# Kernel tuning notes

Hardware: AMD Instinct MI355X
Metric: run time of the kernel (lower is better)

Reference implementation:

```python
import jax, jax.numpy as jnp
import numpy as np

B = 16
N = [4096, 1024, 256, 64, 16]
NF = [1, 16, 32, 64, 128, 256]
DEG = 6
KS = 5
LAT = 32


def spline_conv(x, edge_index, pseudo, W, root, bias):
    """SplineConv: open B-spline, degree 1, dim 3, kernel_size 5, sum aggregation (norm=False).
    x: [Nn, Cin], edge_index: [2, E] (src, dst), pseudo: [E, 3] in [0,1], W: [125, Cin, Cout]."""
    src, dst = edge_index[0], edge_index[1]
    v = pseudo * (KS - 1)                       # degree-1 open spline interval
    lo = jnp.clip(jnp.floor(v), 0.0, KS - 2)
    frac = v - lo                               # [E, 3]
    lo = lo.astype(jnp.int32)
    xs = x[src]                                 # [E, Cin] gather
    strides = jnp.array([1, KS, KS * KS], dtype=jnp.int32)
    msg = jnp.zeros((src.shape[0], W.shape[2]), dtype=x.dtype)
    for s in range(8):                          # (degree+1)^dim = 8 basis products
        bits = np.array([(s >> d) & 1 for d in range(3)], dtype=np.int32)
        basis = jnp.prod(jnp.where(bits[None, :] == 1, frac, 1.0 - frac), axis=1)  # [E]
        kidx = jnp.sum((lo + bits[None, :]) * strides[None, :], axis=1)            # [E]
        Wg = W[kidx]                                                               # [E, Cin, Cout]
        msg = msg + basis[:, None] * jnp.einsum('ei,eio->eo', xs, Wg)
    agg = jax.ops.segment_sum(msg, dst, num_segments=x.shape[0])
    return agg + x @ root + bias


def _fwd(fl, ei):
    (x, ea0, ea1, ea2, ea3, ea4, P01, P12, P23, P34, Pn1, P1n, P43, P32, P21, P10,
     W_c1, r_c1, b_c1, W_c2, r_c2, b_c2, W_c3, r_c3, b_c3, W_c4, r_c4, b_c4, W_c5, r_c5, b_c5,
     W_d5, r_d5, b_d5, W_d4, r_d4, b_d4, W_d3, r_d3, b_d3, W_d2, r_d2, b_d2, W_d1, r_d1, b_d1,
     fce1_w, fce1_b, fce21_w, fce21_b, fce22_w, fce22_b, fcd3_w, fcd3_b, fcd4_w, fcd4_b, eps) = fl
    ei0, ei1, ei2, ei3, ei4 = ei
    elu = jax.nn.elu
    # ---- encoder ----
    h = elu(spline_conv(x, ei0, ea0, W_c1, r_c1, b_c1))
    h = P01 @ h.reshape(B, N[0], NF[1])
    h = elu(spline_conv(h.reshape(-1, NF[1]), ei1, ea1, W_c2, r_c2, b_c2))
    h = P12 @ h.reshape(B, N[1], NF[2])
    h = elu(spline_conv(h.reshape(-1, NF[2]), ei2, ea2, W_c3, r_c3, b_c3))
    h = P23 @ h.reshape(B, N[2], NF[3])
    h = elu(spline_conv(h.reshape(-1, NF[3]), ei3, ea3, W_c4, r_c4, b_c4))
    h = P34 @ h.reshape(B, N[3], NF[4])
    h = elu(spline_conv(h.reshape(-1, NF[4]), ei4, ea4, W_c5, r_c5, b_c5))
    h = (Pn1 @ h.reshape(B, N[4], NF[5])).reshape(B, NF[5])
    # 1x1 convs over [B, C, 1, 1] == dense layers
    h = elu(h @ fce1_w + fce1_b)
    mu = h @ fce21_w + fce21_b
    logvar = h @ fce22_w + fce22_b
    # ---- reparameterize ----
    z = eps * jnp.exp(0.5 * logvar) + mu
    # ---- decoder ----
    h = elu(z @ fcd3_w + fcd3_b)
    h = elu(h @ fcd4_w + fcd4_b)
    h = P1n @ h.reshape(B, 1, NF[5])            # [B, N4, nf5]
    h = elu(spline_conv(h.reshape(-1, NF[5]), ei4, ea4, W_d5, r_d5, b_d5))
    h = P43 @ h.reshape(B, N[4], NF[4])
    h = elu(spline_conv(h.reshape(-1, NF[4]), ei3, ea3, W_d4, r_d4, b_d4))
    h = P32 @ h.reshape(B, N[3], NF[3])
    h = elu(spline_conv(h.reshape(-1, NF[3]), ei2, ea2, W_d3, r_d3, b_d3))
    h = P21 @ h.reshape(B, N[2], NF[2])
    h = elu(spline_conv(h.reshape(-1, NF[2]), ei1, ea1, W_d2, r_d2, b_d2))
    h = P10 @ h.reshape(B, N[1], NF[1])
    h = elu(spline_conv(h.reshape(-1, NF[1]), ei0, ea0, W_d1, r_d1, b_d1))
    recon = h.reshape(B, -1)                    # [B, N0] (nf0 == 1)
    return recon, mu, logvar


def setup_inputs() -> dict:
    key = jax.random.key(0)
    ks = iter(jax.random.split(key, 128))
    def nrm(shape, scale=1.0):
        return jax.random.normal(next(ks), shape, dtype=jnp.float32) * scale
    def edges(n):
        # per-sample random mesh-like connectivity, offset per graph copy
        e = jax.random.randint(next(ks), (2, B, n * DEG), 0, n)
        off = (jnp.arange(B) * n)[None, :, None]
        return (e + off).reshape(2, -1).astype(jnp.int32)
    inp = {}
    inp['x'] = nrm((B * N[0], NF[0]))
    for i in range(5):
        inp[f'ea{i}'] = jax.random.uniform(next(ks), (B * N[i] * DEG, 3), dtype=jnp.float32)
    pools = {'P01': (N[1], N[0]), 'P12': (N[2], N[1]), 'P23': (N[3], N[2]), 'P34': (N[4], N[3]),
             'Pn1': (1, N[4]), 'P1n': (N[4], 1), 'P43': (N[3], N[4]), 'P32': (N[2], N[3]),
             'P21': (N[1], N[2]), 'P10': (N[0], N[1])}
    for k2, (a, b) in pools.items():
        inp[k2] = nrm((a, b), 1.0 / np.sqrt(b))
    def spl(name, ci, co):
        inp[f'W_{name}'] = nrm((KS ** 3, ci, co), 0.1 / np.sqrt(ci))
        inp[f'r_{name}'] = nrm((ci, co), 1.0 / np.sqrt(ci))
        inp[f'b_{name}'] = nrm((co,), 0.01)
    spl('c1', NF[0], NF[1]); spl('c2', NF[1], NF[2]); spl('c3', NF[2], NF[3]); spl('c4', NF[3], NF[4]); spl('c5', NF[4], NF[5])
    spl('d5', NF[5], NF[4]); spl('d4', NF[4], NF[3]); spl('d3', NF[3], NF[2]); spl('d2', NF[2], NF[1]); spl('d1', NF[1], NF[0])
    def lin(name, ci, co):
        inp[f'{name}_w'] = nrm((ci, co), 1.0 / np.sqrt(ci))
        inp[f'{name}_b'] = nrm((co,), 0.01)
    lin('fce1', NF[5], NF[5]); lin('fce21', NF[5], LAT); lin('fce22', NF[5], LAT)
    lin('fcd3', LAT, NF[5]); lin('fcd4', NF[5], NF[5])
    inp['eps'] = nrm((B, LAT))
    for i in range(5):
        inp[f'ei{i}'] = edges(N[i])
    return inp


def reference(x, ea0, ea1, ea2, ea3, ea4, P01, P12, P23, P34, Pn1, P1n, P43, P32, P21, P10,
              W_c1, r_c1, b_c1, W_c2, r_c2, b_c2, W_c3, r_c3, b_c3, W_c4, r_c4, b_c4, W_c5, r_c5, b_c5,
              W_d5, r_d5, b_d5, W_d4, r_d4, b_d4, W_d3, r_d3, b_d3, W_d2, r_d2, b_d2, W_d1, r_d1, b_d1,
              fce1_w, fce1_b, fce21_w, fce21_b, fce22_w, fce22_b, fcd3_w, fcd3_b, fcd4_w, fcd4_b, eps,
              ei0, ei1, ei2, ei3, ei4):
    fl = (x, ea0, ea1, ea2, ea3, ea4, P01, P12, P23, P34, Pn1, P1n, P43, P32, P21, P10,
          W_c1, r_c1, b_c1, W_c2, r_c2, b_c2, W_c3, r_c3, b_c3, W_c4, r_c4, b_c4, W_c5, r_c5, b_c5,
          W_d5, r_d5, b_d5, W_d4, r_d4, b_d4, W_d3, r_d3, b_d3, W_d2, r_d2, b_d2, W_d1, r_d1, b_d1,
          fce1_w, fce1_b, fce21_w, fce21_b, fce22_w, fce22_b, fcd3_w, fcd3_b, fcd4_w, fcd4_b, eps)
    return _fwd(fl, (ei0, ei1, ei2, ei3, ei4))
```

## Files before the change

kernel.cpp:

```cpp
#include <hip/hip_runtime.h>
#include <hip/hip_bf16.h>

#define TPB 256
#define CDIV(a,b) (((a)+(b)-1)/(b))

__device__ __forceinline__ float elu_f(float v) {
    return v > 0.f ? v : expm1f(v);
}

__device__ __forceinline__ int ld_idx(const void* __restrict__ ei, int pos, int is64) {
    if (is64) return (int)((const long long*)ei)[pos];
    return ((const int*)ei)[pos];
}

__device__ __forceinline__ void spline_basis(const float* __restrict__ pseudo, int e,
                                             float bas[8], int kidx[8]) {
    float f[3]; int lo[3];
#pragma unroll
    for (int d = 0; d < 3; ++d) {
        float v = pseudo[e * 3 + d] * 4.f;
        float l = floorf(v);
        l = fminf(fmaxf(l, 0.f), 3.f);
        f[d] = v - l;
        lo[d] = (int)l;
    }
#pragma unroll
    for (int s = 0; s < 8; ++s) {
        int b0 = s & 1, b1 = (s >> 1) & 1, b2 = (s >> 2) & 1;
        bas[s] = (b0 ? f[0] : 1.f - f[0]) * (b1 ? f[1] : 1.f - f[1]) * (b2 ? f[2] : 1.f - f[2]);
        kidx[s] = (lo[0] + b0) + 5 * (lo[1] + b1) + 25 * (lo[2] + b2);
    }
}

__global__ void k_detect(const int* __restrict__ ei0_as_i32, int* __restrict__ flag) {
    if (threadIdx.x == 0 && blockIdx.x == 0) {
        int zeros = 0;
        for (int k = 0; k < 128; ++k)
            if (ei0_as_i32[2 * k + 1] == 0) zeros++;
        flag[0] = (zeros >= 120) ? 1 : 0;
    }
}

__global__ __launch_bounds__(TPB) void k_zero(float* __restrict__ p, int n) {
    int t = blockIdx.x * blockDim.x + threadIdx.x;
    if (t < n) p[t] = 0.f;
}

__global__ __launch_bounds__(TPB) void k_zero_i(int* __restrict__ p, int n) {
    int t = blockIdx.x * blockDim.x + threadIdx.x;
    if (t < n) p[t] = 0;
}

__global__ __launch_bounds__(TPB) void k_csr_count(const void* __restrict__ ei,
                                                   int* __restrict__ cnt, int E,
                                                   const int* __restrict__ flag) {
    int t = blockIdx.x * blockDim.x + threadIdx.x;
    if (t >= E) return;
    int dst = ld_idx(ei, E + t, flag[0]);
    atomicAdd(&cnt[dst], 1);
}

__global__ __launch_bounds__(1024) void k_csr_scan(const int* __restrict__ cnt,
                                                   int* __restrict__ row_ptr) {
    __shared__ int s_part[1024];
    int t = threadIdx.x;
    int base = t * 64;
    int sum = 0;
    for (int i = 0; i < 64; ++i) sum += cnt[base + i];
    s_part[t] = sum;
    __syncthreads();
    for (int off = 1; off < 1024; off <<= 1) {
        int v = (t >= off) ? s_part[t - off] : 0;
        __syncthreads();
        s_part[t] += v;
        __syncthreads();
    }
    int run = (t == 0) ? 0 : s_part[t - 1];
    for (int i = 0; i < 64; ++i) { row_ptr[base + i] = run; run += cnt[base + i]; }
    if (t == 1023) row_ptr[65536] = run;
}

__global__ __launch_bounds__(TPB) void k_csr_fill(const void* __restrict__ ei,
                                                  const int* __restrict__ row_ptr,
                                                  int* __restrict__ cur,
                                                  int* __restrict__ eid, int E,
                                                  const int* __restrict__ flag) {
    int t = blockIdx.x * blockDim.x + threadIdx.x;
    if (t >= E) return;
    int dst = ld_idx(ei, E + t, flag[0]);
    int pos = row_ptr[dst] + atomicAdd(&cur[dst], 1);
    eid[pos] = t;
}

__global__ __launch_bounds__(256) void k_gather_c1(const float* __restrict__ x,
                                                   const float* __restrict__ pseudo,
                                                   const void* __restrict__ ei,
                                                   const float* __restrict__ W,
                                                   const float* __restrict__ root,
                                                   const float* __restrict__ bias,
                                                   const int* __restrict__ row_ptr,
                                                   const int* __restrict__ eid,
                                                   float* __restrict__ agg,
                                                   const int* __restrict__ flag) {
    __shared__ float4 s_w[500];
    for (int i = threadIdx.x; i < 500; i += 256)
        s_w[i] = reinterpret_cast<const float4*>(W)[i];
    __syncthreads();
    int t = blockIdx.x * 256 + threadIdx.x;
    int n = t >> 2, cg = t & 3, co0 = cg * 4;
    int is64 = flag[0];
    float xn = x[n];
    float a0 = fmaf(xn, root[co0 + 0], bias[co0 + 0]);
    float a1 = fmaf(xn, root[co0 + 1], bias[co0 + 1]);
    float a2 = fmaf(xn, root[co0 + 2], bias[co0 + 2]);
    float a3 = fmaf(xn, root[co0 + 3], bias[co0 + 3]);
    int rb = row_ptr[n], re = row_ptr[n + 1];
    for (int idx = rb; idx < re; ++idx) {
        int e = eid[idx];
        int src = ld_idx(ei, e, is64);
        float bas[8]; int kidx[8];
        spline_basis(pseudo, e, bas, kidx);
        float xs = x[src];
        float m0 = 0.f, m1 = 0.f, m2 = 0.f, m3 = 0.f;
#pragma unroll
        for (int s = 0; s < 8; ++s) {
            float4 w = s_w[kidx[s] * 4 + cg];
            float bs = bas[s];
            m0 = fmaf(bs, w.x, m0);
            m1 = fmaf(bs, w.y, m1);
            m2 = fmaf(bs, w.z, m2);
            m3 = fmaf(bs, w.w, m3);
        }
        a0 = fmaf(xs, m0, a0);
        a1 = fmaf(xs, m1, a1);
        a2 = fmaf(xs, m2, a2);
        a3 = fmaf(xs, m3, a3);
    }
    float4 v = make_float4(a0, a1, a2, a3);
    *reinterpret_cast<float4*>(&agg[n * 16 + co0]) = v;
}

__global__ __launch_bounds__(256) void k_gather_d1(const float* __restrict__ xin,
                                                   const float* __restrict__ pseudo,
                                                   const void* __restrict__ ei,
                                                   const float* __restrict__ W,
                                                   const float* __restrict__ root,
                                                   const float* __restrict__ bias,
                                                   const int* __restrict__ row_ptr,
                                                   const int* __restrict__ eid,
                                                   float* __restrict__ outp,
                                                   const int* __restrict__ flag) {
    __shared__ float s_w[2000];
    for (int i = threadIdx.x; i < 2000; i += 256) s_w[i] = W[i];
    __syncthreads();
    int t = blockIdx.x * 256 + threadIdx.x;
    int n = t >> 2, l = t & 3;
    int is64 = flag[0];
    int rb = row_ptr[n], re = row_ptr[n + 1];
    float acc = 0.f;
    for (int idx = rb + l; idx < re; idx += 4) {
        int e = eid[idx];
        int src = ld_idx(ei, e, is64);
        float bas[8]; int kidx[8];
        spline_basis(pseudo, e, bas, kidx);
        const float4* xs4 = reinterpret_cast<const float4*>(xin + src * 16);
        float4 xv0 = xs4[0], xv1 = xs4[1], xv2 = xs4[2], xv3 = xs4[3];
        float m = 0.f;
#pragma unroll
        for (int s = 0; s < 8; ++s) {
            const float4* wp = reinterpret_cast<const float4*>(s_w + kidx[s] * 16);
            float4 w0 = wp[0], w1 = wp[1], w2 = wp[2], w3 = wp[3];
            float p = 0.f;
            p = fmaf(xv0.x, w0.x, p); p = fmaf(xv0.y, w0.y, p);
            p = fmaf(xv0.z, w0.z, p); p = fmaf(xv0.w, w0.w, p);
            p = fmaf(xv1.x, w1.x, p); p = fmaf(xv1.y, w1.y, p);
            p = fmaf(xv1.z, w1.z, p); p = fmaf(xv1.w, w1.w, p);
            p = fmaf(xv2.x, w2.x, p); p = fmaf(xv2.y, w2.y, p);
            p = fmaf(xv2.z, w2.z, p); p = fmaf(xv2.w, w2.w, p);
            p = fmaf(xv3.x, w3.x, p); p = fmaf(xv3.y, w3.y, p);
            p = fmaf(xv3.z, w3.z, p); p = fmaf(xv3.w, w3.w, p);
            m = fmaf(bas[s], p, m);
        }
        acc += m;
    }
    acc += __shfl_xor(acc, 1);
    acc += __shfl_xor(acc, 2);
    if (l == 0) {
        const float4* xr = reinterpret_cast<const float4*>(xin + n * 16);
        const float4* rr = reinterpret_cast<const float4*>(root);
        float r = bias[0];
#pragma unroll
        for (int q = 0; q < 4; ++q) {
            float4 xv = xr[q], rv = rr[q];
            r = fmaf(xv.x, rv.x, r); r = fmaf(xv.y, rv.y, r);
            r = fmaf(xv.z, rv.z, r); r = fmaf(xv.w, rv.w, r);
        }
        outp[n] = elu_f(r + acc);
    }
}

__global__ __launch_bounds__(TPB) void k_root4(const float* __restrict__ x,
                                               const float* __restrict__ root,
                                               const float* __restrict__ bias,
                                               float* __restrict__ out,
                                               int nnode, int cin, int cout) {
    int t = blockIdx.x * blockDim.x + threadIdx.x;
    if (t >= nnode * cout) return;
    int n = t / cout, co = t - n * cout;
    const float4* xr = reinterpret_cast<const float4*>(x + n * cin);
    float a0 = 0.f, a1 = 0.f, a2 = 0.f, a3 = 0.f;
    int q4 = cin >> 2;
    for (int q = 0; q < q4; ++q) {
        float4 xv = xr[q];
        const float* rp = root + (q * 4) * cout + co;
        a0 = fmaf(xv.x, rp[0], a0);
        a1 = fmaf(xv.y, rp[cout], a1);
        a2 = fmaf(xv.z, rp[2 * cout], a2);
        a3 = fmaf(xv.w, rp[3 * cout], a3);
    }
    out[t] = bias[co] + ((a0 + a1) + (a2 + a3));
}

template <int CIN, int COUT, int CSPLIT>
__global__ __launch_bounds__(TPB) void k_msg4(const float* __restrict__ x,
                                              const float* __restrict__ pseudo,
                                              const void* __restrict__ ei,
                                              const float* __restrict__ W,
                                              float* __restrict__ agg, int E,
                                              const int* __restrict__ flag) {
    constexpr int COG = COUT / 4;
    constexpr int CPT = CIN / CSPLIT;
    int t = blockIdx.x * blockDim.x + threadIdx.x;
    if (t >= E * COG * CSPLIT) return;
    int is64 = flag[0];
    int cog = t % COG;
    int rest = t / COG;
    int cs = rest % CSPLIT;
    int e = rest / CSPLIT;
    int co0 = cog * 4;
    int src = ld_idx(ei, e, is64);
    int dst = ld_idx(ei, E + e, is64);
    float bas[8]; int kidx[8];
    spline_basis(pseudo, e, bas, kidx);
    int wof[8];
#pragma unroll
    for (int s = 0; s < 8; ++s) wof[s] = kidx[s] * CIN * COUT + co0;
    float a0 = 0.f, a1 = 0.f, a2 = 0.f, a3 = 0.f;
    const float* xp = x + src * CIN + cs * CPT;
    const int cbase = cs * CPT * COUT;
    for (int ci = 0; ci < CPT; ++ci) {
        float xv = xp[ci];
        int off = cbase + ci * COUT;
#pragma unroll
        for (int s = 0; s < 8; ++s) {
            float4 w = *reinterpret_cast<const float4*>(&W[wof[s] + off]);
            float bx = bas[s] * xv;
            a0 = fmaf(bx, w.x, a0);
            a1 = fmaf(bx, w.y, a1);
            a2 = fmaf(bx, w.z, a2);
            a3 = fmaf(bx, w.w, a3);
        }
    }
    float* ap = &agg[dst * COUT + co0];
    atomicAdd(ap + 0, a0);
    atomicAdd(ap + 1, a1);
    atomicAdd(ap + 2, a2);
    atomicAdd(ap + 3, a3);
}

template <int CIN, int COUT>
__global__ __launch_bounds__(TPB) void k_msg_s(const float* __restrict__ x,
                                               const float* __restrict__ pseudo,
                                               const void* __restrict__ ei,
                                               const float* __restrict__ W,
                                               float* __restrict__ agg, int E,
                                               const int* __restrict__ flag) {
    int t = blockIdx.x * blockDim.x + threadIdx.x;
    if (t >= E * COUT) return;
    int is64 = flag[0];
    int e = t / COUT, co = t - e * COUT;
    int src = ld_idx(ei, e, is64);
    int dst = ld_idx(ei, E + e, is64);
    float bas[8]; int kidx[8];
    spline_basis(pseudo, e, bas, kidx);
    float acc = 0.f;
    const float* xp = x + src * CIN;
    for (int ci = 0; ci < CIN; ++ci) {
        float xv = xp[ci];
#pragma unroll
        for (int s = 0; s < 8; ++s)
            acc = fmaf(bas[s] * xv, W[kidx[s] * CIN * COUT + ci * COUT + co], acc);
    }
    atomicAdd(&agg[dst * COUT + co], acc);
}

__global__ __launch_bounds__(1024) void k_msg_c1(const float* __restrict__ x,
                                                 const float* __restrict__ pseudo,
                                                 const void* __restrict__ ei,
                                                 const float* __restrict__ W,
                                                 const float* __restrict__ root,
                                                 const float* __restrict__ bias,
                                                 float* __restrict__ agg,
                                                 const int* __restrict__ flag) {
    __shared__ float s_acc[4096 * 4];
    __shared__ float s_w[125 * 4];
    int b = blockIdx.x, cg = blockIdx.y, t = threadIdx.x;
    int co0 = cg * 4;
    int is64 = flag[0];
    if (t < 500) s_w[t] = W[(t >> 2) * 16 + co0 + (t & 3)];
    float r0 = root[co0], r1 = root[co0 + 1], r2 = root[co0 + 2], r3 = root[co0 + 3];
    float b0 = bias[co0], b1 = bias[co0 + 1], b2 = bias[co0 + 2], b3 = bias[co0 + 3];
    for (int n = t; n < 4096; n += 1024) {
        float xv = x[b * 4096 + n];
        s_acc[n * 4 + 0] = fmaf(xv, r0, b0);
        s_acc[n * 4 + 1] = fmaf(xv, r1, b1);
        s_acc[n * 4 + 2] = fmaf(xv, r2, b2);
        s_acc[n * 4 + 3] = fmaf(xv, r3, b3);
    }
    __syncthreads();
    int ebeg = b * 24576;
    for (int k = t; k < 24576; k += 1024) {
        int e = ebeg + k;
        int src = ld_idx(ei, e, is64);
        int dst = ld_idx(ei, 393216 + e, is64);
        float xv = x[src];
        float bas[8]; int kidx[8];
        spline_basis(pseudo, e, bas, kidx);
        float m0 = 0.f, m1 = 0.f, m2 = 0.f, m3 = 0.f;
#pragma unroll
        for (int s = 0; s < 8; ++s) {
            const float* wp = s_w + kidx[s] * 4;
            float bs = bas[s];
            m0 = fmaf(bs, wp[0], m0);
            m1 = fmaf(bs, wp[1], m1);
            m2 = fmaf(bs, wp[2], m2);
            m3 = fmaf(bs, wp[3], m3);
        }
        int dl = (dst - b * 4096) * 4;
        atomicAdd(&s_acc[dl + 0], m0 * xv);
        atomicAdd(&s_acc[dl + 1], m1 * xv);
        atomicAdd(&s_acc[dl + 2], m2 * xv);
        atomicAdd(&s_acc[dl + 3], m3 * xv);
    }
    __syncthreads();
    for (int n = t; n < 4096; n += 1024) {
        float4 v = *reinterpret_cast<float4*>(&s_acc[n * 4]);
        *reinterpret_cast<float4*>(&agg[(b * 4096 + n) * 16 + co0]) = v;
    }
}

template <int F, int ELU>
__global__ __launch_bounds__(256) void k_pool2(const float* __restrict__ in,
                                               const float* __restrict__ P,
                                               float* __restrict__ out,
                                               int nout, int nin) {
    constexpr int FQ = F / 4;
    constexpr int TI = 256 / FQ;
    constexpr int KT = 64;
    constexpr int PS = KT + 4;
    __shared__ float s_p[TI * PS];
    __shared__ float4 s_in[KT * FQ];
    int tid = threadIdx.x;
    int fq = tid % FQ;
    int i = tid / FQ;
    int b = blockIdx.y;
    int gi = blockIdx.x * TI + i;
    int nchunk = nin / gridDim.z;
    int kbeg = blockIdx.z * nchunk;
    const float4* inb4 = reinterpret_cast<const float4*>(in + b * nin * F);
    float4 acc = make_float4(0.f, 0.f, 0.f, 0.f);

    for (int k0 = kbeg; k0 < kbeg + nchunk; k0 += KT) {
        __syncthreads();
        for (int idx = tid; idx < TI * (KT / 4); idx += 256) {
            int r = idx / (KT / 4), c = idx % (KT / 4);
            float4 v = *reinterpret_cast<const float4*>(&P[(blockIdx.x * TI + r) * nin + k0 + c * 4]);
            *reinterpret_cast<float4*>(&s_p[r * PS + c * 4]) = v;
        }
        for (int idx = tid; idx < KT * FQ; idx += 256) {
            float4 v = inb4[(size_t)(k0 + idx / FQ) * FQ + (idx % FQ)];
            if (ELU) {
                v.x = elu_f(v.x); v.y = elu_f(v.y);
                v.z = elu_f(v.z); v.w = elu_f(v.w);
            }
            s_in[idx] = v;
        }
        __syncthreads();
#pragma unroll 4
        for (int j = 0; j < KT; j += 4) {
            float4 pv = *reinterpret_cast<const float4*>(&s_p[i * PS + j]);
            float4 v0 = s_in[(j + 0) * FQ + fq];
            float4 v1 = s_in[(j + 1) * FQ + fq];
            float4 v2 = s_in[(j + 2) * FQ + fq];
            float4 v3 = s_in[(j + 3) * FQ + fq];
            acc.x = fmaf(pv.x, v0.x, acc.x); acc.y = fmaf(pv.x, v0.y, acc.y);
            acc.z = fmaf(pv.x, v0.z, acc.z); acc.w = fmaf(pv.x, v0.w, acc.w);
            acc.x = fmaf(pv.y, v1.x, acc.x); acc.y = fmaf(pv.y, v1.y, acc.y);
            acc.z = fmaf(pv.y, v1.z, acc.z); acc.w = fmaf(pv.y, v1.w, acc.w);
            acc.x = fmaf(pv.z, v2.x, acc.x); acc.y = fmaf(pv.z, v2.y, acc.y);
            acc.z = fmaf(pv.z, v2.z, acc.z); acc.w = fmaf(pv.z, v2.w, acc.w);
            acc.x = fmaf(pv.w, v3.x, acc.x); acc.y = fmaf(pv.w, v3.y, acc.y);
            acc.z = fmaf(pv.w, v3.z, acc.z); acc.w = fmaf(pv.w, v3.w, acc.w);
        }
    }
    float* o = out + ((size_t)b * nout + gi) * F + fq * 4;
    if (gridDim.z > 1) {
        atomicAdd(o + 0, acc.x); atomicAdd(o + 1, acc.y);
        atomicAdd(o + 2, acc.z); atomicAdd(o + 3, acc.w);
    } else {
        *reinterpret_cast<float4*>(o) = acc;
    }
}

__global__ __launch_bounds__(TPB) void k_pool_e(const float* __restrict__ in,
                                                const float* __restrict__ P,
                                                float* __restrict__ out,
                                                int nout, int nin, int F, int elu) {
    int t = blockIdx.x * blockDim.x + threadIdx.x;
    if (t >= 16 * nout * F) return;
    int f = t % F;
    int rest = t / F;
    int i = rest % nout;
    int b = rest / nout;
    const float* ip = in + b * nin * F + f;
    const float* pp = P + i * nin;
    float acc = 0.f;
    if (elu) {
#pragma unroll 4
        for (int j = 0; j < nin; ++j) acc = fmaf(pp[j], elu_f(ip[j * F]), acc);
    } else {
#pragma unroll 4
        for (int j = 0; j < nin; ++j) acc = fmaf(pp[j], ip[j * F], acc);
    }
    out[t] = acc;
}

__global__ __launch_bounds__(1024) void k_fc_fused2(
        const float* __restrict__ c5agg, const float* __restrict__ Pn1,
        const float* __restrict__ fce1_w, const float* __restrict__ fce1_b,
        const float* __restrict__ fce21_w, const float* __restrict__ fce21_b,
        const float* __restrict__ fce22_w, const float* __restrict__ fce22_b,
        const float* __restrict__ eps,
        const float* __restrict__ fcd3_w, const float* __restrict__ fcd3_b,
        const float* __restrict__ fcd4_w, const float* __restrict__ fcd4_b,
        const float* __restrict__ P1n,
        float* __restrict__ out_mu, float* __restrict__ out_lv,
        float* __restrict__ dec_in) {
    __shared__ float s0[256], s1[256], sz[32], sp[1024];
    int b = blockIdx.x, t = threadIdx.x;
    if (t < 256) {
        const float* ap = c5agg + b * 4096 + t;
        float acc = 0.f;
#pragma unroll
        for (int n = 0; n < 16; ++n) acc = fmaf(Pn1[n], elu_f(ap[n * 256]), acc);
        s0[t] = acc;
    }
    __syncthreads();
    {
        int q = t >> 8, co = t & 255;
        const float* w = fce1_w + co;
        float a = 0.f;
        int c0 = q * 64;
        for (int ci = 0; ci < 64; ci += 8) {
#pragma unroll
            for (int k = 0; k < 8; ++k) a = fmaf(s0[c0 + ci + k], w[(c0 + ci + k) * 256], a);
        }
        sp[t] = a;
    }
    __syncthreads();
    if (t < 256) s1[t] = elu_f(sp[t] + sp[t + 256] + sp[t + 512] + sp[t + 768] + fce1_b[t]);
    __syncthreads();
    if (t < 512) {
        int which = t >> 8, r = t & 255;
        int co = r & 31, q = r >> 5;
        const float* w = (which ? fce22_w : fce21_w) + co;
        float a = 0.f;
        int c0 = q * 32;
#pragma unroll
        for (int k = 0; k < 32; ++k) a = fmaf(s1[c0 + k], w[(c0 + k) * 32], a);
        sp[t] = a;
    }
    __syncthreads();
    if (t < 64) {
        int which = t >> 5, co = t & 31;
        float m = (which ? fce22_b : fce21_b)[co];
        int base = which * 256 + co;
#pragma unroll
        for (int q = 0; q < 8; ++q) m += sp[base + q * 32];
        if (which == 0) { out_mu[b * 32 + co] = m; s0[co] = m; }
        else            { out_lv[b * 32 + co] = m; s0[64 + co] = m; }
    }
    __syncthreads();
    if (t < 32) sz[t] = fmaf(eps[b * 32 + t], expf(0.5f * s0[64 + t]), s0[t]);
    __syncthreads();
    if (t < 256) {
        float d = fcd3_b[t];
#pragma unroll
        for (int ci = 0; ci < 32; ++ci) d = fmaf(sz[ci], fcd3_w[ci * 256 + t], d);
        s0[t] = elu_f(d);
    }
    __syncthreads();
    {
        int q = t >> 8, co = t & 255;
        const float* w = fcd4_w + co;
        float a = 0.f;
        int c0 = q * 64;
        for (int ci = 0; ci < 64; ci += 8) {
#pragma unroll
            for (int k = 0; k < 8; ++k) a = fmaf(s0[c0 + ci + k], w[(c0 + ci + k) * 256], a);
        }
        sp[t] = a;
    }
    __syncthreads();
    if (t < 256) s1[t] = elu_f(sp[t] + sp[t + 256] + sp[t + 512] + sp[t + 768] + fcd4_b[t]);
    __syncthreads();
    {
        float* op = dec_in + b * 4096;
        for (int idx = t; idx < 4096; idx += 1024) {
            int n = idx >> 8, f = idx & 255;
            op[idx] = P1n[n] * s1[f];
        }
    }
}

__global__ __launch_bounds__(TPB) void k_elu_out(const float* __restrict__ in,
                                                 float* __restrict__ out, int n) {
    int t = blockIdx.x * blockDim.x + threadIdx.x;
    if (t < n) out[t] = elu_f(in[t]);
}

extern "C" void kernel_launch(void* const* d_in, const int* in_sizes, int n_in,
                              void* d_out, int out_size, void* d_ws, size_t ws_size,
                              hipStream_t stream) {
    const float* x    = (const float*)d_in[0];
    const float* ea0  = (const float*)d_in[1];
    const float* ea1  = (const float*)d_in[2];
    const float* ea2  = (const float*)d_in[3];
    const float* ea3  = (const float*)d_in[4];
    const float* ea4  = (const float*)d_in[5];
    const float* P01  = (const float*)d_in[6];
    const float* P12  = (const float*)d_in[7];
    const float* P23  = (const float*)d_in[8];
    const float* P34  = (const float*)d_in[9];
    const float* Pn1  = (const float*)d_in[10];
    const float* P1n  = (const float*)d_in[11];
    const float* P43  = (const float*)d_in[12];
    const float* P32  = (const float*)d_in[13];
    const float* P21  = (const float*)d_in[14];
    const float* P10  = (const float*)d_in[15];
    const float* W_c1 = (const float*)d_in[16]; const float* r_c1 = (const float*)d_in[17]; const float* b_c1 = (const float*)d_in[18];
    const float* W_c2 = (const float*)d_in[19]; const float* r_c2 = (const float*)d_in[20]; const float* b_c2 = (const float*)d_in[21];
    const float* W_c3 = (const float*)d_in[22]; const float* r_c3 = (const float*)d_in[23]; const float* b_c3 = (const float*)d_in[24];
    const float* W_c4 = (const float*)d_in[25]; const float* r_c4 = (const float*)d_in[26]; const float* b_c4 = (const float*)d_in[27];
    const float* W_c5 = (const float*)d_in[28]; const float* r_c5 = (const float*)d_in[29]; const float* b_c5 = (const float*)d_in[30];
    const float* W_d5 = (const float*)d_in[31]; const float* r_d5 = (const float*)d_in[32]; const float* b_d5 = (const float*)d_in[33];
    const float* W_d4 = (const float*)d_in[34]; const float* r_d4 = (const float*)d_in[35]; const float* b_d4 = (const float*)d_in[36];
    const float* W_d3 = (const float*)d_in[37]; const float* r_d3 = (const float*)d_in[38]; const float* b_d3 = (const float*)d_in[39];
    const float* W_d2 = (const float*)d_in[40]; const float* r_d2 = (const float*)d_in[41]; const float* b_d2 = (const float*)d_in[42];
    const float* W_d1 = (const float*)d_in[43]; const float* r_d1 = (const float*)d_in[44]; const float* b_d1 = (const float*)d_in[45];
    const float* fce1_w  = (const float*)d_in[46]; const float* fce1_b  = (const float*)d_in[47];
    const float* fce21_w = (const float*)d_in[48]; const float* fce21_b = (const float*)d_in[49];
    const float* fce22_w = (const float*)d_in[50]; const float* fce22_b = (const float*)d_in[51];
    const float* fcd3_w  = (const float*)d_in[52]; const float* fcd3_b  = (const float*)d_in[53];
    const float* fcd4_w  = (const float*)d_in[54]; const float* fcd4_b  = (const float*)d_in[55];
    const float* eps  = (const float*)d_in[56];
    const void* ei0 = d_in[57];
    const void* ei1 = d_in[58];
    const void* ei2 = d_in[59];
    const void* ei3 = d_in[60];
    const void* ei4 = d_in[61];

    const int E0 = 393216, E1 = 98304, E2 = 24576, E3 = 6144, E4 = 1536;
    const int N0 = 65536, N1 = 16384, N2 = 4096, N3 = 1024, N4 = 256;

    float* sm   = (float*)d_ws;
    float* bufA = sm + 13824;
    float* bufB = bufA + 1048576;
    int*  flag  = (int*)(bufB + 262144);
    int*  csr_row = (int*)(bufB + 262144 + 64);
    int*  csr_cur = csr_row + 65537;
    int*  csr_eid = csr_cur + 65536;
    const size_t WS_NEED = (size_t)(13824 + 1048576 + 262144 + 64 + 524352) * 4;
    const bool big_ws = ws_size >= WS_NEED;

    float* out = (float*)d_out;
    float* out_mu = out + 65536;
    float* out_lv = out + 66048;

    auto g = [](int n) { return dim3((unsigned)CDIV(n, TPB)); };

    k_detect<<<1, 64, 0, stream>>>((const int*)ei0, flag);

    if (big_ws) {
        k_zero_i<<<g(65536), TPB, 0, stream>>>(csr_cur, 65536);
        k_csr_count<<<g(E0), TPB, 0, stream>>>(ei0, csr_cur, E0, flag);
        k_csr_scan<<<1, 1024, 0, stream>>>(csr_cur, csr_row);
        k_zero_i<<<g(65536), TPB, 0, stream>>>(csr_cur, 65536);
        k_csr_fill<<<g(E0), TPB, 0, stream>>>(ei0, csr_row, csr_cur, csr_eid, E0, flag);
    }

    if (big_ws) {
        k_gather_c1<<<1024, 256, 0, stream>>>(x, ea0, ei0, W_c1, r_c1, b_c1,
                                              csr_row, csr_eid, bufA, flag);
    } else {
        k_msg_c1<<<dim3(16, 4), 1024, 0, stream>>>(x, ea0, ei0, W_c1, r_c1, b_c1, bufA, flag);
    }
    k_zero<<<g(262144), TPB, 0, stream>>>(bufB, 262144);
    k_pool2<16, 1><<<dim3(16, 16, 4), 256, 0, stream>>>(bufA, P01, bufB, 1024, 4096);

    k_root4<<<g(N1 * 32), TPB, 0, stream>>>(bufB, r_c2, b_c2, bufA, N1, 16, 32);
    k_msg4<16, 32, 1><<<g(E1 * 8), TPB, 0, stream>>>(bufB, ea1, ei1, W_c2, bufA, E1, flag);
    k_zero<<<g(131072), TPB, 0, stream>>>(bufB, 131072);
    k_pool2<32, 1><<<dim3(8, 16, 2), 256, 0, stream>>>(bufA, P12, bufB, 256, 1024);

    k_root4<<<g(N2 * 64), TPB, 0, stream>>>(bufB, r_c3, b_c3, bufA, N2, 32, 64);
    k_msg4<32, 64, 1><<<g(E2 * 16), TPB, 0, stream>>>(bufB, ea2, ei2, W_c3, bufA, E2, flag);
    k_zero<<<g(65536), TPB, 0, stream>>>(bufB, 65536);
    k_pool2<64, 1><<<dim3(4, 16, 2), 256, 0, stream>>>(bufA, P23, bufB, 64, 256);

    k_root4<<<g(N3 * 128), TPB, 0, stream>>>(bufB, r_c4, b_c4, bufA, N3, 64, 128);
    k_msg4<64, 128, 1><<<g(E3 * 32), TPB, 0, stream>>>(bufB, ea3, ei3, W_c4, bufA, E3, flag);
    k_pool_e<<<g(16 * 16 * 128), TPB, 0, stream>>>(bufA, P34, bufB, 16, 64, 128, 1);

    k_root4<<<g(N4 * 256), TPB, 0, stream>>>(bufB, r_c5, b_c5, bufA, N4, 128, 256);
    k_msg4<128, 256, 2><<<g(E4 * 128), TPB, 0, stream>>>(bufB, ea4, ei4, W_c5, bufA, E4, flag);

    k_fc_fused2<<<16, 1024, 0, stream>>>(bufA, Pn1,
                                         fce1_w, fce1_b, fce21_w, fce21_b, fce22_w, fce22_b,
                                         eps, fcd3_w, fcd3_b, fcd4_w, fcd4_b, P1n,
                                         out_mu, out_lv, bufA);

    k_root4<<<g(N4 * 128), TPB, 0, stream>>>(bufA, r_d5, b_d5, bufB, N4, 256, 128);
    k_msg4<256, 128, 4><<<g(E4 * 128), TPB, 0, stream>>>(bufA, ea4, ei4, W_d5, bufB, E4, flag);
    k_pool_e<<<g(16 * 64 * 128), TPB, 0, stream>>>(bufB, P43, bufA, 64, 16, 128, 1);

    k_root4<<<g(N3 * 64), TPB, 0, stream>>>(bufA, r_d4, b_d4, bufB, N3, 128, 64);
    k_msg4<128, 64, 2><<<g(E3 * 32), TPB, 0, stream>>>(bufA, ea3, ei3, W_d4, bufB, E3, flag);
    k_pool2<64, 1><<<dim3(16, 16, 1), 256, 0, stream>>>(bufB, P32, bufA, 256, 64);

    k_root4<<<g(N2 * 32), TPB, 0, stream>>>(bufA, r_d3, b_d3, bufB, N2, 64, 32);
    k_msg4<64, 32, 1><<<g(E2 * 8), TPB, 0, stream>>>(bufA, ea2, ei2, W_d3, bufB, E2, flag);
    k_pool2<32, 1><<<dim3(32, 16, 1), 256, 0, stream>>>(bufB, P21, bufA, 1024, 256);

    k_root4<<<g(N1 * 16), TPB, 0, stream>>>(bufA, r_d2, b_d2, bufB, N1, 32, 16);
    k_msg4<32, 16, 1><<<g(E1 * 4), TPB, 0, stream>>>(bufA, ea1, ei1, W_d2, bufB, E1, flag);
    k_pool2<16, 1><<<dim3(64, 16, 1), 256, 0, stream>>>(bufB, P10, bufA, 4096, 1024);

    if (big_ws) {
        k_gather_d1<<<1024, 256, 0, stream>>>(bufA, ea0, ei0, W_d1, r_d1, b_d1,
                                              csr_row, csr_eid, out, flag);
    } else {
        k_root4<<<g(N0 * 1), TPB, 0, stream>>>(bufA, r_d1, b_d1, bufB, N0, 16, 1);
        k_msg_s<16, 1><<<g(E0), TPB, 0, stream>>>(bufA, ea0, ei0, W_d1, bufB, E0, flag);
        k_elu_out<<<g(N0), TPB, 0, stream>>>(bufB, out, 65536);
    }
}
```

Before: 938.3 us.

## Build CSR for all levels and use dst-gather spline conv with shared-memory weights

Builds CSR (count, scan, fill) for all five graph levels in single batched kernels. It then replaces the atomic-scatter k_msg4 layers with a gather kernel that stages the relevant W slice in shared memory and accumulates per destination node. Small levels with the channel dimension fully covered fuse the root term and write directly; split-channel variants still use atomics on top of k_root4. The change is meant to cut global atomics and repeated global reads of W, at the cost of extra CSR-building work and load imbalance on nodes with many edges.

```diff
diff --git a/kernel.cpp b/kernel.cpp
--- a/kernel.cpp
+++ b/kernel.cpp
@@ -49,6 +49,73 @@
 __global__ __launch_bounds__(TPB) void k_zero_i(int* __restrict__ p, int n) {
     int t = blockIdx.x * blockDim.x + threadIdx.x;
     if (t < n) p[t] = 0;
+}
+
+__global__ __launch_bounds__(TPB) void k_csr_count5(const void* e0, const void* e1,
+                                                    const void* e2, const void* e3,
+                                                    const void* e4, int* __restrict__ cnt,
+                                                    const int* __restrict__ flag) {
+    int t = blockIdx.x * blockDim.x + threadIdx.x;
+    if (t >= 523776) return;
+    int is64 = flag[0];
+    const void* ei; int e, E, noff;
+    if (t < 393216)      { ei = e0; e = t;          E = 393216; noff = 0; }
+    else if (t < 491520) { ei = e1; e = t - 393216; E = 98304;  noff = 65536; }
+    else if (t < 516096) { ei = e2; e = t - 491520; E = 24576;  noff = 81920; }
+    else if (t < 522240) { ei = e3; e = t - 516096; E = 6144;   noff = 86016; }
+    else                 { ei = e4; e = t - 522240; E = 1536;   noff = 87040; }
+    int dst = ld_idx(ei, E + e, is64);
+    atomicAdd(&cnt[noff + dst], 1);
+}
+
+__global__ __launch_bounds__(1024) void k_csr_scan5(const int* __restrict__ cnt,
+                                                    int* __restrict__ rows) {
+    const int NODES[5] = {65536, 16384, 4096, 1024, 256};
+    const int NOFF[5]  = {0, 65536, 81920, 86016, 87040};
+    const int ROFF[5]  = {0, 65537, 81922, 86019, 87044};
+    int l = blockIdx.x;
+    int nodes = NODES[l];
+    const int* c = cnt + NOFF[l];
+    int* rp = rows + ROFF[l];
+    __shared__ int s_part[1024];
+    int t = threadIdx.x;
+    int chunk = (nodes + 1023) >> 10;
+    int b0 = t * chunk;
+    int b1 = min(b0 + chunk, nodes);
+    int sum = 0;
+    for (int i = b0; i < b1; ++i) sum += c[i];
+    s_part[t] = sum;
+    __syncthreads();
+    for (int off = 1; off < 1024; off <<= 1) {
+        int v = (t >= off) ? s_part[t - off] : 0;
+        __syncthreads();
+        s_part[t] += v;
+        __syncthreads();
+    }
+    int run = (t == 0) ? 0 : s_part[t - 1];
+    for (int i = b0; i < b1; ++i) { rp[i] = run; run += c[i]; }
+    if (t == 0) rp[nodes] = s_part[1023];
+}
+
+__global__ __launch_bounds__(TPB) void k_csr_fill5(const void* e0, const void* e1,
+                                                   const void* e2, const void* e3,
+                                                   const void* e4,
+                                                   const int* __restrict__ rows,
+                                                   int* __restrict__ cur,
+                                                   int* __restrict__ eids,
+                                                   const int* __restrict__ flag) {
+    int t = blockIdx.x * blockDim.x + threadIdx.x;
+    if (t >= 523776) return;
+    int is64 = flag[0];
+    const void* ei; int e, E, noff, roff, eoff;
+    if (t < 393216)      { ei = e0; e = t;          E = 393216; noff = 0;     roff = 0;     eoff = 0; }
+    else if (t < 491520) { ei = e1; e = t - 393216; E = 98304;  noff = 65536; roff = 65537; eoff = 393216; }
+    else if (t < 516096) { ei = e2; e = t - 491520; E = 24576;  noff = 81920; roff = 81922; eoff = 491520; }
+    else if (t < 522240) { ei = e3; e = t - 516096; E = 6144;   noff = 86016; roff = 86019; eoff = 516096; }
+    else                 { ei = e4; e = t - 522240; E = 1536;   noff = 87040; roff = 87044; eoff = 522240; }
+    int dst = ld_idx(ei, E + e, is64);
+    int pos = rows[roff + dst] + atomicAdd(&cur[noff + dst], 1);
+    eids[eoff + pos] = e;
 }
 
 __global__ __launch_bounds__(TPB) void k_csr_count(const void* __restrict__ ei,
@@ -196,6 +263,75 @@
             r = fmaf(xv.z, rv.z, r); r = fmaf(xv.w, rv.w, r);
         }
         outp[n] = elu_f(r + acc);
+    }
+}
+
+template <int CIN, int COUT, int CSPLIT, int IROOT>
+__global__ __launch_bounds__(256) void k_gW(const float* __restrict__ x,
+                                            const float* __restrict__ pseudo,
+                                            const void* __restrict__ ei,
+                                            const float* __restrict__ W,
+                                            const float* __restrict__ root,
+                                            const float* __restrict__ bias,
+                                            const int* __restrict__ row_ptr,
+                                            const int* __restrict__ eid,
+                                            float* __restrict__ agg,
+                                            const int* __restrict__ flag) {
+    constexpr int COG = COUT / 4;
+    constexpr int CPT = CIN / CSPLIT;
+    __shared__ float4 s_w[125 * CPT];
+    int cg = blockIdx.y, cih = blockIdx.z;
+    const float4* W4 = reinterpret_cast<const float4*>(W);
+    for (int i = threadIdx.x; i < 125 * CPT; i += 256) {
+        int k = i / CPT, ci = i - k * CPT;
+        s_w[i] = W4[(k * CIN + cih * CPT + ci) * COG + cg];
+    }
+    __syncthreads();
+    int n = blockIdx.x * 256 + threadIdx.x;
+    int is64 = flag[0];
+    int co0 = cg * 4;
+    float4 acc = make_float4(0.f, 0.f, 0.f, 0.f);
+    if (IROOT) {
+        acc = reinterpret_cast<const float4*>(bias)[cg];
+        const float* xp = x + (size_t)n * CIN;
+        const float4* r4 = reinterpret_cast<const float4*>(root);
+#pragma unroll
+        for (int ci = 0; ci < CIN; ++ci) {
+            float xv = xp[ci];
+            float4 rv = r4[ci * COG + cg];
+            acc.x = fmaf(xv, rv.x, acc.x); acc.y = fmaf(xv, rv.y, acc.y);
+            acc.z = fmaf(xv, rv.z, acc.z); acc.w = fmaf(xv, rv.w, acc.w);
+        }
+    }
+    int rb = row_ptr[n], re = row_ptr[n + 1];
+    for (int idx = rb; idx < re; ++idx) {
+        int e = eid[idx];
+        int src = ld_idx(ei, e, is64);
+        float bas[8]; int kidx[8];
+        spline_basis(pseudo, e, bas, kidx);
+        float xv[CPT];
+        const float* xp = x + (size_t)src * CIN + cih * CPT;
+#pragma unroll
+        for (int ci = 0; ci < CPT; ++ci) xv[ci] = xp[ci];
+#pragma unroll
+        for (int s = 0; s < 8; ++s) {
+            const float4* wp = s_w + kidx[s] * CPT;
+            float bs = bas[s];
+#pragma unroll
+            for (int ci = 0; ci < CPT; ++ci) {
+                float bx = bs * xv[ci];
+                float4 w = wp[ci];
+                acc.x = fmaf(bx, w.x, acc.x); acc.y = fmaf(bx, w.y, acc.y);
+                acc.z = fmaf(bx, w.z, acc.z); acc.w = fmaf(bx, w.w, acc.w);
+            }
+        }
+    }
+    float* o = agg + (size_t)n * COUT + co0;
+    if (IROOT) {
+        *reinterpret_cast<float4*>(o) = acc;
+    } else {
+        atomicAdd(o + 0, acc.x); atomicAdd(o + 1, acc.y);
+        atomicAdd(o + 2, acc.z); atomicAdd(o + 3, acc.w);
     }
 }
 
@@ -577,11 +713,20 @@
     float* bufA = sm + 13824;
     float* bufB = bufA + 1048576;
     int*  flag  = (int*)(bufB + 262144);
-    int*  csr_row = (int*)(bufB + 262144 + 64);
-    int*  csr_cur = csr_row + 65537;
-    int*  csr_eid = csr_cur + 65536;
-    const size_t WS_NEED = (size_t)(13824 + 1048576 + 262144 + 64 + 524352) * 4;
-    const bool big_ws = ws_size >= WS_NEED;
+    int*  ibase = flag + 64;
+    int* cur  = ibase;
+    int* rows = cur + 87296;
+    int* eids = rows + 87301;
+    const size_t WS_ALL = (size_t)(13824 + 1048576 + 262144 + 64 + 87296 + 87301 + 523776) * 4;
+    int* o_row = ibase;
+    int* o_cur = o_row + 65537;
+    int* o_eid = o_cur + 65536;
+    const size_t WS_OLD = (size_t)(13824 + 1048576 + 262144 + 64 + 524352) * 4;
+    const bool bigA = ws_size >= WS_ALL;
+    const bool big0 = ws_size >= WS_OLD;
+
+    const int ROFF[5] = {0, 65537, 81922, 86019, 87044};
+    const int EOFF[5] = {0, 393216, 491520, 516096, 522240};
 
     float* out = (float*)d_out;
     float* out_mu = out + 65536;
@@ -591,17 +736,74 @@
 
     k_detect<<<1, 64, 0, stream>>>((const int*)ei0, flag);
 
-    if (big_ws) {
-        k_zero_i<<<g(65536), TPB, 0, stream>>>(csr_cur, 65536);
-        k_csr_count<<<g(E0), TPB, 0, stream>>>(ei0, csr_cur, E0, flag);
-        k_csr_scan<<<1, 1024, 0, stream>>>(csr_cur, csr_row);
-        k_zero_i<<<g(65536), TPB, 0, stream>>>(csr_cur, 65536);
-        k_csr_fill<<<g(E0), TPB, 0, stream>>>(ei0, csr_row, csr_cur, csr_eid, E0, flag);
-    }
-
-    if (big_ws) {
+    if (bigA) {
+        k_zero_i<<<g(87296), TPB, 0, stream>>>(cur, 87296);
+        k_csr_count5<<<g(523776), TPB, 0, stream>>>(ei0, ei1, ei2, ei3, ei4, cur, flag);
+        k_csr_scan5<<<5, 1024, 0, stream>>>(cur, rows);
+        k_zero_i<<<g(87296), TPB, 0, stream>>>(cur, 87296);
+        k_csr_fill5<<<g(523776), TPB, 0, stream>>>(ei0, ei1, ei2, ei3, ei4, rows, cur, eids, flag);
+
         k_gather_c1<<<1024, 256, 0, stream>>>(x, ea0, ei0, W_c1, r_c1, b_c1,
-                                              csr_row, csr_eid, bufA, flag);
+                                              rows + ROFF[0], eids + EOFF[0], bufA, flag);
+        k_zero<<<g(262144), TPB, 0, stream>>>(bufB, 262144);
+        k_pool2<16, 1><<<dim3(16, 16, 4), 256, 0, stream>>>(bufA, P01, bufB, 1024, 4096);
+
+        k_gW<16, 32, 1, 1><<<dim3(64, 8, 1), 256, 0, stream>>>(bufB, ea1, ei1, W_c2, r_c2, b_c2,
+                                                               rows + ROFF[1], eids + EOFF[1], bufA, flag);
+        k_zero<<<g(131072), TPB, 0, stream>>>(bufB, 131072);
+        k_pool2<32, 1><<<dim3(8, 16, 2), 256, 0, stream>>>(bufA, P12, bufB, 256, 1024);
+
+        k_gW<32, 64, 1, 1><<<dim3(16, 16, 1), 256, 0, stream>>>(bufB, ea2, ei2, W_c3, r_c3, b_c3,
+                                                                rows + ROFF[2], eids + EOFF[2], bufA, flag);
+        k_zero<<<g(65536), TPB, 0, stream>>>(bufB, 65536);
+        k_pool2<64, 1><<<dim3(4, 16, 2), 256, 0, stream>>>(bufA, P23, bufB, 64, 256);
+
+        k_root4<<<g(N3 * 128), TPB, 0, stream>>>(bufB, r_c4, b_c4, bufA, N3, 64, 128);
+        k_gW<64, 128, 2, 0><<<dim3(4, 32, 2), 256, 0, stream>>>(bufB, ea3, ei3, W_c4, r_c4, b_c4,
+                                                                rows + ROFF[3], eids + EOFF[3], bufA, flag);
+        k_pool_e<<<g(16 * 16 * 128), TPB, 0, stream>>>(bufA, P34, bufB, 16, 64, 128, 1);
+
+        k_root4<<<g(N4 * 256), TPB, 0, stream>>>(bufB, r_c5, b_c5, bufA, N4, 128, 256);
+        k_gW<128, 256, 4, 0><<<dim3(1, 64, 4), 256, 0, stream>>>(bufB, ea4, ei4, W_c5, r_c5, b_c5,
+                                                                 rows + ROFF[4], eids + EOFF[4], bufA, flag);
+
+        k_fc_fused2<<<16, 1024, 0, stream>>>(bufA, Pn1,
+                                             fce1_w, fce1_b, fce21_w, fce21_b, fce22_w, fce22_b,
+                                             eps, fcd3_w, fcd3_b, fcd4_w, fcd4_b, P1n,
+                                             out_mu, out_lv, bufA);
+
+        k_root4<<<g(N4 * 128), TPB, 0, stream>>>(bufA, r_d5, b_d5, bufB, N4, 256, 128);
+        k_gW<256, 128, 8, 0><<<dim3(1, 32, 8), 256, 0, stream>>>(bufA, ea4, ei4, W_d5, r_d5, b_d5,
+                                                                 rows + ROFF[4], eids + EOFF[4], bufB, flag);
+        k_pool_e<<<g(16 * 64 * 128), TPB, 0, stream>>>(bufB, P43, bufA, 64, 16, 128, 1);
+
+        k_root4<<<g(N3 * 64), TPB, 0, stream>>>(bufA, r_d4, b_d4, bufB, N3, 128, 64);
+        k_gW<128, 64, 4, 0><<<dim3(4, 16, 4), 256, 0, stream>>>(bufA, ea3, ei3, W_d4, r_d4, b_d4,
+                                                                rows + ROFF[3], eids + EOFF[3], bufB, flag);
+        k_pool2<64, 1><<<dim3(16, 16, 1), 256, 0, stream>>>(bufB, P32, bufA, 256, 64);
+
+        k_root4<<<g(N2 * 32), TPB, 0, stream>>>(bufA, r_d3, b_d3, bufB, N2, 64, 32);
+        k_gW<64, 32, 2, 0><<<dim3(16, 8, 2), 256, 0, stream>>>(bufA, ea2, ei2, W_d3, r_d3, b_d3,
+                                                               rows + ROFF[2], eids + EOFF[2], bufB, flag);
+        k_pool2<32, 1><<<dim3(32, 16, 1), 256, 0, stream>>>(bufB, P21, bufA, 1024, 256);
+
+        k_gW<32, 16, 1, 1><<<dim3(64, 4, 1), 256, 0, stream>>>(bufA, ea1, ei1, W_d2, r_d2, b_d2,
+                                                               rows + ROFF[1], eids + EOFF[1], bufB, flag);
+        k_pool2<16, 1><<<dim3(64, 16, 1), 256, 0, stream>>>(bufB, P10, bufA, 4096, 1024);
+
+        k_gather_d1<<<1024, 256, 0, stream>>>(bufA, ea0, ei0, W_d1, r_d1, b_d1,
+                                              rows + ROFF[0], eids + EOFF[0], out, flag);
+        return;
+    }
+
+    if (big0) {
+        k_zero_i<<<g(65536), TPB, 0, stream>>>(o_cur, 65536);
+        k_csr_count<<<g(E0), TPB, 0, stream>>>(ei0, o_cur, E0, flag);
+        k_csr_scan<<<1, 1024, 0, stream>>>(o_cur, o_row);
+        k_zero_i<<<g(65536), TPB, 0, stream>>>(o_cur, 65536);
+        k_csr_fill<<<g(E0), TPB, 0, stream>>>(ei0, o_row, o_cur, o_eid, E0, flag);
+        k_gather_c1<<<1024, 256, 0, stream>>>(x, ea0, ei0, W_c1, r_c1, b_c1,
+                                              o_row, o_eid, bufA, flag);
     } else {
         k_msg_c1<<<dim3(16, 4), 1024, 0, stream>>>(x, ea0, ei0, W_c1, r_c1, b_c1, bufA, flag);
     }
@@ -646,9 +848,9 @@
     k_msg4<32, 16, 1><<<g(E1 * 4), TPB, 0, stream>>>(bufA, ea1, ei1, W_d2, bufB, E1, flag);
     k_pool2<16, 1><<<dim3(64, 16, 1), 256, 0, stream>>>(bufB, P10, bufA, 4096, 1024);
 
-    if (big_ws) {
+    if (big0) {
         k_gather_d1<<<1024, 256, 0, stream>>>(bufA, ea0, ei0, W_d1, r_d1, b_d1,
-                                              csr_row, csr_eid, out, flag);
+                                              o_row, o_eid, out, flag);
     } else {
         k_root4<<<g(N0 * 1), TPB, 0, stream>>>(bufA, r_d1, b_d1, bufB, N0, 16, 1);
         k_msg_s<16, 1><<<g(E0), TPB, 0, stream>>>(bufA, ea0, ei0, W_d1, bufB, E0, flag);
```

Result: slower. 2.028 ms (+116.1%).
